# Performance work log

Hardware: AMD Instinct MI355X
Metric: run time of the kernel (lower is better)

Reference implementation:

```python
import jax, jax.numpy as jnp
import numpy as np

CAT_CARDS = [10, 20, 15, 8, 30, 12, 5, 25, 6, 40, 18, 9]   # categorical_card entries with card > 1 (first 20 entries)
NUM = 32          # num_numerical
NBIN = 8          # categorical_card[:-2] entries with card == 1
NLIKE = 2         # last two categorical_card entries, both card 1
NMASK = NUM + len(CAT_CARDS) + NBIN + NLIKE   # 32 + 22 = 54 mask heads
LAT, HID, B = 128, 1024, 16384
TAU = 1.0
EPS = 1e-20


def setup_inputs() -> dict:
    key = jax.random.key(0)
    ks = jax.random.split(key, 7)
    w = lambda k, sh: (jax.random.normal(k, sh, jnp.float32) * 0.02)
    return {
        "z": jax.random.normal(ks[0], (B, LAT), jnp.float32),
        "W1": w(ks[1], (LAT, HID)), "b1": jnp.zeros((HID,), jnp.float32),
        "W_num": w(ks[2], (HID, NUM)), "b_num": jnp.zeros((NUM,), jnp.float32),
        "W_cat": w(ks[3], (HID, sum(CAT_CARDS))), "b_cat": jnp.zeros((sum(CAT_CARDS),), jnp.float32),
        "W_bin": w(ks[4], (HID, NBIN)), "b_bin": jnp.zeros((NBIN,), jnp.float32),
        "W_like": w(ks[5], (HID, NLIKE)), "b_like": jnp.zeros((NLIKE,), jnp.float32),
        "W_mask": w(ks[6], (HID, NMASK)), "b_mask": jnp.zeros((NMASK,), jnp.float32),
    }


def _gumbel_sigmoid(logits, key, tau=TAU):
    # matches torch: noise~U(0,1); g = -log(-log(noise+eps)+eps); sigmoid((logits+g)/tau); hard=False
    u = jax.random.uniform(key, logits.shape, logits.dtype)
    g = -jnp.log(-jnp.log(u + EPS) + EPS)
    return jax.nn.sigmoid((logits + g) / tau)


def reference(z, W1, b1, W_num, b_num, W_cat, b_cat, W_bin, b_bin, W_like, b_like, W_mask, b_mask):
    nk = jax.random.split(jax.random.key(1), 3)
    h = jax.nn.relu(z @ W1 + b1)                       # [B, HID]
    num_out = h @ W_num + b_num                        # [B, NUM]

    cat_logits = h @ W_cat + b_cat                     # [B, sum(cards)] fused GEMM, then split per head
    splits = np.cumsum(CAT_CARDS)[:-1].tolist()
    cat_out = tuple(jnp.split(cat_logits, splits, axis=1))

    # use_gumbel=True, hard=False: binary / likewise / mask heads get gumbel-sigmoid
    bin_out = _gumbel_sigmoid(h @ W_bin + b_bin, nk[0])      # [B, NBIN]
    like_out = _gumbel_sigmoid(h @ W_like + b_like, nk[1])   # [B, NLIKE]
    mask_out = _gumbel_sigmoid(h @ W_mask + b_mask, nk[2])   # [B, NMASK]

    bins = tuple(bin_out[:, i:i + 1] for i in range(NBIN))
    likes = tuple(like_out[:, i:i + 1] for i in range(NLIKE))
    masks = tuple(mask_out[:, i:i + 1] for i in range(NMASK))
    return (num_out,) + cat_out + bins + likes + masks
```

## Files before the change

kernel.cpp:

```cpp
#include <hip/hip_runtime.h>
#include <stdint.h>

#define B_ROWS 16384
#define LATD   128
#define HIDD   1024

typedef __bf16 bf16x8 __attribute__((ext_vector_type(8)));
typedef float  f32x4  __attribute__((ext_vector_type(4)));
typedef float  f32x4v __attribute__((ext_vector_type(4)));
typedef unsigned short ushort8v __attribute__((ext_vector_type(8)));
typedef unsigned int   uint2v   __attribute__((ext_vector_type(2)));

template<int N> __device__ __forceinline__ void waitv() {
  asm volatile("s_waitcnt vmcnt(%0)" :: "i"(N) : "memory");
  __builtin_amdgcn_sched_barrier(0);
}
__device__ __forceinline__ void gl16(bf16x8& r, const unsigned short* p) {
  asm volatile("global_load_dwordx4 %0, %1, off" : "=v"(r) : "v"(p));
}
template<int OFF> __device__ __forceinline__ void gl16o(bf16x8& r, const unsigned short* p) {
  asm volatile("global_load_dwordx4 %0, %1, off offset:%2" : "=v"(r) : "v"(p), "i"(OFF));
}
#define LGKM_BARRIER() do {                                        \
    asm volatile("s_waitcnt lgkmcnt(0)" ::: "memory");             \
    __builtin_amdgcn_s_barrier();                                  \
    asm volatile("" ::: "memory");                                 \
  } while (0)

struct TF2 { unsigned int a, b; };

#define TF_R(x0,x1,r) { x0 += x1; x1 = ((x1 << (r)) | (x1 >> (32 - (r)))); x1 ^= x0; }

__host__ __device__ constexpr TF2 threefry2x32(unsigned k0, unsigned k1, unsigned c0, unsigned c1) {
  unsigned ks2 = k0 ^ k1 ^ 0x1BD11BDAu;
  unsigned x0 = c0 + k0, x1 = c1 + k1;
  TF_R(x0,x1,13) TF_R(x0,x1,15) TF_R(x0,x1,26) TF_R(x0,x1,6)
  x0 += k1;  x1 += ks2 + 1u;
  TF_R(x0,x1,17) TF_R(x0,x1,29) TF_R(x0,x1,16) TF_R(x0,x1,24)
  x0 += ks2; x1 += k0 + 2u;
  TF_R(x0,x1,13) TF_R(x0,x1,15) TF_R(x0,x1,26) TF_R(x0,x1,6)
  x0 += k0;  x1 += k1 + 3u;
  TF_R(x0,x1,17) TF_R(x0,x1,29) TF_R(x0,x1,16) TF_R(x0,x1,24)
  x0 += k1;  x1 += ks2 + 4u;
  TF_R(x0,x1,13) TF_R(x0,x1,15) TF_R(x0,x1,26) TF_R(x0,x1,6)
  x0 += ks2; x1 += k0 + 5u;
  return {x0, x1};
}

constexpr TF2 NK0 = threefry2x32(0u, 1u, 0u, 0u);
constexpr TF2 NK1 = threefry2x32(0u, 1u, 0u, 1u);
constexpr TF2 NK2 = threefry2x32(0u, 1u, 0u, 2u);

__device__ __forceinline__ unsigned short f2bf(float f) {
  unsigned u = __float_as_uint(f);
  return (unsigned short)((u + 0x7fffu + ((u >> 16) & 1u)) >> 16);
}

__global__ __launch_bounds__(256) void prep_kernel(
    const float* __restrict__ W1,
    const float* __restrict__ Wnum, const float* __restrict__ Wcat,
    const float* __restrict__ Wbin, const float* __restrict__ Wlike,
    const float* __restrict__ Wmask,
    const float* __restrict__ bnum, const float* __restrict__ bcat,
    const float* __restrict__ bbin, const float* __restrict__ blike,
    const float* __restrict__ bmask,
    unsigned short* __restrict__ W1p,
    unsigned short* __restrict__ Wallp,
    float* __restrict__ ball) {
  __shared__ __align__(16) unsigned short lds[16 * 136];
  const int b = blockIdx.x, t = threadIdx.x;

  if (b < 64) {
    const int n0 = b * 16;
    const int nq = t & 15;
    float v[8];
    #pragma unroll
    for (int i = 0; i < 8; ++i) {
      int k = i * 16 + (t >> 4);
      v[i] = W1[(size_t)k * HIDD + n0 + nq];
    }
    #pragma unroll
    for (int i = 0; i < 8; ++i) {
      int k = i * 16 + (t >> 4);
      lds[nq * 136 + k] = f2bf(v[i]);
    }
    __syncthreads();
    const int ks = t >> 6, l = t & 63;
    const int l15 = l & 15, l4 = (l >> 4);
    ushort8v p = *(const ushort8v*)(lds + l15 * 136 + ks * 32 + l4 * 8);
    *(ushort8v*)(W1p + ((size_t)(b * 4 + ks) * 64 + l) * 8) = p;
  } else if (b < 224) {
    const int q  = b - 64;
    const int nt = q >> 3, kb = q & 7;
    const int n0 = nt * 16, k0 = kb * 128;
    const int n = n0 + (t & 15);
    const float* src = nullptr; int stride = 0;
    if (n < 32)       { src = Wnum  + n;         stride = 32;  }
    else if (n < 230) { src = Wcat  + (n - 32);  stride = 198; }
    else if (n < 238) { src = Wbin  + (n - 230); stride = 8;   }
    else if (n < 240) { src = Wlike + (n - 238); stride = 2;   }
    else if (n < 294) { src = Wmask + (n - 240); stride = 54;  }
    float v[8];
    if (src) {
      #pragma unroll
      for (int i = 0; i < 8; ++i) {
        int kk_loc = i * 16 + (t >> 4);
        v[i] = src[(size_t)(k0 + kk_loc) * stride];
      }
    } else {
      #pragma unroll
      for (int i = 0; i < 8; ++i) v[i] = 0.f;
    }
    #pragma unroll
    for (int i = 0; i < 8; ++i) {
      int kk_loc = i * 16 + (t >> 4);
      lds[(t & 15) * 136 + kk_loc] = f2bf(v[i]);
    }
    __syncthreads();
    const int kt_loc = t >> 6, l = t & 63;
    const int l15 = l & 15, l4 = (l >> 4);
    ushort8v p = *(const ushort8v*)(lds + l15 * 136 + kt_loc * 32 + l4 * 8);
    const int g = nt * 32 + kb * 4 + kt_loc;
    *(ushort8v*)(Wallp + ((size_t)g * 64 + l) * 8) = p;
  } else {
    for (int n = t; n < 320; n += 256) {
      float v = 0.f;
      if (n < 32)       v = bnum [n];
      else if (n < 230) v = bcat [n - 32];
      else if (n < 238) v = bbin [n - 230];
      else if (n < 240) v = blike[n - 238];
      else if (n < 294) v = bmask[n - 240];
      ball[n] = v;
    }
  }
}

template<int G>
__device__ __forceinline__ void run_phases(
    const int w, const int lane, const int l15, const int l4, const int nt0,
    const unsigned short* __restrict__ W1p, const unsigned short* __restrict__ Wallp,
    const float* __restrict__ b1,
    unsigned char* smem, f32x4 (&acc)[4][3]) {

  unsigned short* zs = (unsigned short*)smem;
  unsigned char* hbase  = smem + 17408;
  unsigned char* mytile = hbase + w * 16384;

  f32x4 hb1[8];
  #pragma unroll
  for (int ct = 0; ct < 8; ++ct)
    hb1[ct] = *(const f32x4*)(b1 + w * 128 + ct * 16 + l4 * 4);

  bf16x8 za[4][4];
  #pragma unroll
  for (int rt = 0; rt < 4; ++rt)
    #pragma unroll
    for (int ks = 0; ks < 4; ++ks)
      za[rt][ks] = *(const bf16x8*)(zs + (rt * 16 + l15) * 136 + ks * 32 + l4 * 8);

  bf16x8 wq1[2][4];
  const unsigned short* w1b = W1p + (size_t)w * 16384 + lane * 8;
  #pragma unroll
  for (int ct = 0; ct < 2; ++ct) {
    const unsigned short* p = w1b + ct * 2048;
    gl16o<0>(wq1[ct][0], p); gl16o<1024>(wq1[ct][1], p);
    gl16o<2048>(wq1[ct][2], p); gl16o<3072>(wq1[ct][3], p);
  }

  bf16x8 wq2[4][G];
  const unsigned short* w2b = Wallp + lane * 8;

  #pragma unroll
  for (int ct = 0; ct < 8; ++ct) {
    if (ct < 7) waitv<4>();
    else        waitv<G * 4>();
    f32x4 a[4] = {};
    #pragma unroll
    for (int ks = 0; ks < 4; ++ks)
      #pragma unroll
      for (int rt = 0; rt < 4; ++rt)
        a[rt] = __builtin_amdgcn_mfma_f32_16x16x32_bf16(wq1[ct & 1][ks], za[rt][ks], a[rt], 0, 0, 0);
    #pragma unroll
    for (int rt = 0; rt < 4; ++rt) {
      float v0 = fmaxf(a[rt][0] + hb1[ct][0], 0.f);
      float v1 = fmaxf(a[rt][1] + hb1[ct][1], 0.f);
      float v2 = fmaxf(a[rt][2] + hb1[ct][2], 0.f);
      float v3 = fmaxf(a[rt][3] + hb1[ct][3], 0.f);
      uint2v u;
      u[0] = (unsigned)f2bf(v0) | ((unsigned)f2bf(v1) << 16);
      u[1] = (unsigned)f2bf(v2) | ((unsigned)f2bf(v3) << 16);
      const int byte = ((ct >> 1) * 4 + rt) * 1024
                     + ((ct & 1) * 2 + (l4 >> 1)) * 256
                     + l15 * 16 + (l4 & 1) * 8;
      *(uint2v*)(mytile + byte) = u;
    }
    if (ct < 6) {
      const unsigned short* p = w1b + (ct + 2) * 2048;
      gl16o<0>(wq1[ct & 1][0], p); gl16o<1024>(wq1[ct & 1][1], p);
      gl16o<2048>(wq1[ct & 1][2], p); gl16o<3072>(wq1[ct & 1][3], p);
    } else if (ct == 6) {
      #pragma unroll
      for (int g = 0; g < 4; ++g)
        #pragma unroll
        for (int cc = 0; cc < G; ++cc)
          gl16(wq2[g][cc], w2b + (size_t)((nt0 + cc) * 32 + g) * 512);
    }
  }

  LGKM_BARRIER();

  #pragma unroll
  for (int rt = 0; rt < 4; ++rt)
    #pragma unroll
    for (int ct = 0; ct < 3; ++ct)
      acc[rt][ct] = (f32x4){0.f, 0.f, 0.f, 0.f};

  #pragma unroll
  for (int g = 0; g < 32; ++g) {
    if (g < 29)       waitv<G * 3>();
    else if (g == 29) waitv<G * 2>();
    else if (g == 30) waitv<G>();
    else              waitv<0>();
    const unsigned char* hc = hbase + (g >> 2) * 16384 + (g & 3) * 4096 + lane * 16;
    #pragma unroll
    for (int rt = 0; rt < 4; ++rt) {
      bf16x8 ha = *(const bf16x8*)(hc + rt * 1024);
      #pragma unroll
      for (int ct = 0; ct < G; ++ct)
        acc[rt][ct] = __builtin_amdgcn_mfma_f32_16x16x32_bf16(ha, wq2[g & 3][ct], acc[rt][ct], 0, 0, 0);
    }
    if (g + 4 < 32) {
      #pragma unroll
      for (int cc = 0; cc < G; ++cc)
        gl16(wq2[g & 3][cc], w2b + (size_t)((nt0 + cc) * 32 + (g + 4)) * 512);
    }
  }
}

__global__ __launch_bounds__(512, 2) void decoder_kernel(
    const float* __restrict__ z, const float* __restrict__ b1,
    const unsigned short* __restrict__ W1p, const unsigned short* __restrict__ Wallp,
    const float* __restrict__ ball, float* __restrict__ out) {
  __shared__ __align__(16) unsigned char smem[148480];
  unsigned short* zs = (unsigned short*)smem;
  float* outs = (float*)smem;

  const int tid  = threadIdx.x;
  const int lane = tid & 63;
  const int w    = tid >> 6;
  const int l15  = lane & 15;
  const int l4   = lane >> 4;
  const int r0   = blockIdx.x * 64;

  #pragma unroll
  for (int it = 0; it < 2; ++it) {
    int ch  = tid + it * 512;
    int row = ch >> 4;
    int k0  = (ch & 15) * 8;
    const float* src = z + (size_t)(r0 + row) * LATD + k0;
    f32x4v f0 = __builtin_nontemporal_load((const f32x4v*)src);
    f32x4v f1 = __builtin_nontemporal_load((const f32x4v*)(src + 4));
    ushort8v p;
    p[0] = f2bf(f0[0]); p[1] = f2bf(f0[1]); p[2] = f2bf(f0[2]); p[3] = f2bf(f0[3]);
    p[4] = f2bf(f1[0]); p[5] = f2bf(f1[1]); p[6] = f2bf(f1[2]); p[7] = f2bf(f1[3]);
    *(ushort8v*)(zs + row * 136 + k0) = p;
  }
  __syncthreads();

  const int cb  = (w < 4) ? w * 48 : 192 + (w - 4) * 32;
  const int nt0 = (w < 4) ? w * 3  : 12 + (w - 4) * 2;
  const int myG = (w < 4) ? 3 : 2;

  f32x4 acc[4][3];
  if (w < 4) run_phases<3>(w, lane, l15, l4, nt0, W1p, Wallp, b1, smem, acc);
  else       run_phases<2>(w, lane, l15, l4, nt0, W1p, Wallp, b1, smem, acc);

  __syncthreads();

  #pragma unroll
  for (int ct = 0; ct < 3; ++ct) {
    if (ct < myG) {
      float b2 = ball[cb + ct * 16 + l15];
      #pragma unroll
      for (int rt = 0; rt < 4; ++rt)
        #pragma unroll
        for (int j = 0; j < 4; ++j)
          outs[(rt * 16 + l4 * 4 + j) * 321 + cb + ct * 16 + l15] = acc[rt][ct][j] + b2;
    }
  }
  __syncthreads();

  {
    constexpr int cards[13] = {32,10,20,15,8,30,12,5,25,6,40,18,9};
    constexpr int cbase[13] = {0,32,42,62,77,85,115,127,132,157,163,203,221};
    #pragma unroll
    for (int blk = 0; blk < 13; ++blk) {
      const int card = cards[blk];
      const int cbs  = cbase[blk];
      float* gout = out + (size_t)B_ROWS * cbs + (size_t)r0 * card;
      for (int v = tid; v < card * 16; v += 512) {
        int gg = v * 4;
        f32x4v vbuf;
        #pragma unroll
        for (int e = 0; e < 4; ++e) {
          int ge = gg + e;
          int brow = ge / card;
          int j = ge - brow * card;
          vbuf[e] = outs[brow * 321 + cbs + j];
        }
        __builtin_nontemporal_store(vbuf, (f32x4v*)(gout + gg));
      }
    }
  }

  {
    int c = 230 + (tid >> 3);
    unsigned ka, kb; int Nh, head;
    if (c < 238)      { ka = NK0.a; kb = NK0.b; Nh = 8;  head = c - 230; }
    else if (c < 240) { ka = NK1.a; kb = NK1.b; Nh = 2;  head = c - 238; }
    else              { ka = NK2.a; kb = NK2.b; Nh = 54; head = c - 240; }
    #pragma unroll
    for (int q = 0; q < 2; ++q) {
      int rq = (tid & 7) * 4 + q * 32;
      f32x4v vbuf;
      #pragma unroll
      for (int e = 0; e < 4; ++e) {
        int rl = rq + e;
        float x = outs[rl * 321 + c];
        unsigned j = (unsigned)((r0 + rl) * Nh + head);
        TF2 t = threefry2x32(ka, kb, 0u, j);
        unsigned bits = t.a ^ t.b;
        float u  = __uint_as_float((bits >> 9) | 0x3f800000u) - 1.0f;
        float gn = -__logf(-__logf(u + 1e-20f) + 1e-20f);
        vbuf[e] = 1.0f / (1.0f + __expf(-(x + gn)));
      }
      __builtin_nontemporal_store(vbuf, (f32x4v*)(out + (size_t)B_ROWS * c + r0 + rq));
    }
  }
}

extern "C" void kernel_launch(void* const* d_in, const int* in_sizes, int n_in,
                              void* d_out, int out_size, void* d_ws, size_t ws_size,
                              hipStream_t stream) {
  const float* z     = (const float*)d_in[0];
  const float* W1    = (const float*)d_in[1];
  const float* b1    = (const float*)d_in[2];
  const float* Wnum  = (const float*)d_in[3];
  const float* bnum  = (const float*)d_in[4];
  const float* Wcat  = (const float*)d_in[5];
  const float* bcat  = (const float*)d_in[6];
  const float* Wbin  = (const float*)d_in[7];
  const float* bbin  = (const float*)d_in[8];
  const float* Wlike = (const float*)d_in[9];
  const float* blike = (const float*)d_in[10];
  const float* Wmask = (const float*)d_in[11];
  const float* bmask = (const float*)d_in[12];

  unsigned short* W1p   = (unsigned short*)d_ws;
  unsigned short* Wallp = W1p + 131072;
  float*          ball  = (float*)(Wallp + 327680);

  prep_kernel<<<225, 256, 0, stream>>>(
      W1, Wnum, Wcat, Wbin, Wlike, Wmask, bnum, bcat, bbin, blike, bmask,
      W1p, Wallp, ball);

  decoder_kernel<<<B_ROWS / 64, 512, 0, stream>>>(
      z, b1, W1p, Wallp, ball, (float*)d_out);
}
```

Measured before the change: 29.33 us.

## Split second GEMM across warps by K halves with LDS reduction

The second GEMM's 320 output columns were split unevenly across 8 warps (3 or 2 column tiles each). Now 4 column groups each own 5 tiles, and the two warp halves each take half of the K dimension. The partial sums are combined through shared memory: one half writes with bias and the other adds after a barrier. This balances MFMA work across warps and halves each warp's K loop. In exchange it adds register pressure from 20 accumulators and 20 prefetch registers, plus an extra barrier and an LDS read-modify-write pass.

```diff
diff --git a/kernel.cpp b/kernel.cpp
--- a/kernel.cpp
+++ b/kernel.cpp
@@ -135,15 +135,43 @@
   }
 }
 
-template<int G>
-__device__ __forceinline__ void run_phases(
-    const int w, const int lane, const int l15, const int l4, const int nt0,
+__global__ __launch_bounds__(512, 2) void decoder_kernel(
+    const float* __restrict__ z, const float* __restrict__ b1,
     const unsigned short* __restrict__ W1p, const unsigned short* __restrict__ Wallp,
-    const float* __restrict__ b1,
-    unsigned char* smem, f32x4 (&acc)[4][3]) {
-
+    const float* __restrict__ ball, float* __restrict__ out) {
+  __shared__ __align__(16) unsigned char smem[148480];
   unsigned short* zs = (unsigned short*)smem;
-  unsigned char* hbase  = smem + 17408;
+  unsigned char* hbase = smem + 17408;
+  float* outs = (float*)smem;
+
+  const int tid  = threadIdx.x;
+  const int lane = tid & 63;
+  const int w    = tid >> 6;
+  const int wc   = w & 3;
+  const int wk   = w >> 2;
+  const int l15  = lane & 15;
+  const int l4   = lane >> 4;
+  const int r0   = blockIdx.x * 64;
+
+  #pragma unroll
+  for (int it = 0; it < 2; ++it) {
+    int ch  = tid + it * 512;
+    int row = ch >> 4;
+    int k0  = (ch & 15) * 8;
+    const float* src = z + (size_t)(r0 + row) * LATD + k0;
+    f32x4v f0 = __builtin_nontemporal_load((const f32x4v*)src);
+    f32x4v f1 = __builtin_nontemporal_load((const f32x4v*)(src + 4));
+    ushort8v p;
+    p[0] = f2bf(f0[0]); p[1] = f2bf(f0[1]); p[2] = f2bf(f0[2]); p[3] = f2bf(f0[3]);
+    p[4] = f2bf(f1[0]); p[5] = f2bf(f1[1]); p[6] = f2bf(f1[2]); p[7] = f2bf(f1[3]);
+    *(ushort8v*)(zs + row * 136 + k0) = p;
+  }
+  __syncthreads();
+
+  const int cb  = wc * 80;
+  const int nt0 = wc * 5;
+  const int kt0 = wk * 16;
+
   unsigned char* mytile = hbase + w * 16384;
 
   f32x4 hb1[8];
@@ -167,13 +195,13 @@
     gl16o<2048>(wq1[ct][2], p); gl16o<3072>(wq1[ct][3], p);
   }
 
-  bf16x8 wq2[4][G];
+  bf16x8 wq2[4][5];
   const unsigned short* w2b = Wallp + lane * 8;
 
   #pragma unroll
   for (int ct = 0; ct < 8; ++ct) {
     if (ct < 7) waitv<4>();
-    else        waitv<G * 4>();
+    else        waitv<20>();
     f32x4 a[4] = {};
     #pragma unroll
     for (int ks = 0; ks < 4; ++ks)
@@ -202,84 +230,48 @@
       #pragma unroll
       for (int g = 0; g < 4; ++g)
         #pragma unroll
-        for (int cc = 0; cc < G; ++cc)
-          gl16(wq2[g][cc], w2b + (size_t)((nt0 + cc) * 32 + g) * 512);
+        for (int cc = 0; cc < 5; ++cc)
+          gl16(wq2[g][cc], w2b + (size_t)((nt0 + cc) * 32 + kt0 + g) * 512);
     }
   }
 
   LGKM_BARRIER();
 
+  f32x4 acc[4][5];
   #pragma unroll
   for (int rt = 0; rt < 4; ++rt)
     #pragma unroll
-    for (int ct = 0; ct < 3; ++ct)
+    for (int ct = 0; ct < 5; ++ct)
       acc[rt][ct] = (f32x4){0.f, 0.f, 0.f, 0.f};
 
   #pragma unroll
-  for (int g = 0; g < 32; ++g) {
-    if (g < 29)       waitv<G * 3>();
-    else if (g == 29) waitv<G * 2>();
-    else if (g == 30) waitv<G>();
-    else              waitv<0>();
-    const unsigned char* hc = hbase + (g >> 2) * 16384 + (g & 3) * 4096 + lane * 16;
+  for (int g = 0; g < 16; ++g) {
+    const int rem = 15 - g;
+    if (rem >= 3)      waitv<15>();
+    else if (rem == 2) waitv<10>();
+    else if (rem == 1) waitv<5>();
+    else               waitv<0>();
+    const int kt = kt0 + g;
+    const unsigned char* hc = hbase + (kt >> 2) * 16384 + (kt & 3) * 4096 + lane * 16;
     #pragma unroll
     for (int rt = 0; rt < 4; ++rt) {
       bf16x8 ha = *(const bf16x8*)(hc + rt * 1024);
       #pragma unroll
-      for (int ct = 0; ct < G; ++ct)
+      for (int ct = 0; ct < 5; ++ct)
         acc[rt][ct] = __builtin_amdgcn_mfma_f32_16x16x32_bf16(ha, wq2[g & 3][ct], acc[rt][ct], 0, 0, 0);
     }
-    if (g + 4 < 32) {
-      #pragma unroll
-      for (int cc = 0; cc < G; ++cc)
-        gl16(wq2[g & 3][cc], w2b + (size_t)((nt0 + cc) * 32 + (g + 4)) * 512);
-    }
-  }
-}
-
-__global__ __launch_bounds__(512, 2) void decoder_kernel(
-    const float* __restrict__ z, const float* __restrict__ b1,
-    const unsigned short* __restrict__ W1p, const unsigned short* __restrict__ Wallp,
-    const float* __restrict__ ball, float* __restrict__ out) {
-  __shared__ __align__(16) unsigned char smem[148480];
-  unsigned short* zs = (unsigned short*)smem;
-  float* outs = (float*)smem;
-
-  const int tid  = threadIdx.x;
-  const int lane = tid & 63;
-  const int w    = tid >> 6;
-  const int l15  = lane & 15;
-  const int l4   = lane >> 4;
-  const int r0   = blockIdx.x * 64;
-
-  #pragma unroll
-  for (int it = 0; it < 2; ++it) {
-    int ch  = tid + it * 512;
-    int row = ch >> 4;
-    int k0  = (ch & 15) * 8;
-    const float* src = z + (size_t)(r0 + row) * LATD + k0;
-    f32x4v f0 = __builtin_nontemporal_load((const f32x4v*)src);
-    f32x4v f1 = __builtin_nontemporal_load((const f32x4v*)(src + 4));
-    ushort8v p;
-    p[0] = f2bf(f0[0]); p[1] = f2bf(f0[1]); p[2] = f2bf(f0[2]); p[3] = f2bf(f0[3]);
-    p[4] = f2bf(f1[0]); p[5] = f2bf(f1[1]); p[6] = f2bf(f1[2]); p[7] = f2bf(f1[3]);
-    *(ushort8v*)(zs + row * 136 + k0) = p;
-  }
+    if (g + 4 < 16) {
+      #pragma unroll
+      for (int cc = 0; cc < 5; ++cc)
+        gl16(wq2[g & 3][cc], w2b + (size_t)((nt0 + cc) * 32 + kt0 + g + 4) * 512);
+    }
+  }
+
   __syncthreads();
 
-  const int cb  = (w < 4) ? w * 48 : 192 + (w - 4) * 32;
-  const int nt0 = (w < 4) ? w * 3  : 12 + (w - 4) * 2;
-  const int myG = (w < 4) ? 3 : 2;
-
-  f32x4 acc[4][3];
-  if (w < 4) run_phases<3>(w, lane, l15, l4, nt0, W1p, Wallp, b1, smem, acc);
-  else       run_phases<2>(w, lane, l15, l4, nt0, W1p, Wallp, b1, smem, acc);
-
-  __syncthreads();
-
-  #pragma unroll
-  for (int ct = 0; ct < 3; ++ct) {
-    if (ct < myG) {
+  if (wk == 0) {
+    #pragma unroll
+    for (int ct = 0; ct < 5; ++ct) {
       float b2 = ball[cb + ct * 16 + l15];
       #pragma unroll
       for (int rt = 0; rt < 4; ++rt)
@@ -287,6 +279,16 @@
         for (int j = 0; j < 4; ++j)
           outs[(rt * 16 + l4 * 4 + j) * 321 + cb + ct * 16 + l15] = acc[rt][ct][j] + b2;
     }
+  }
+  __syncthreads();
+  if (wk == 1) {
+    #pragma unroll
+    for (int ct = 0; ct < 5; ++ct)
+      #pragma unroll
+      for (int rt = 0; rt < 4; ++rt)
+        #pragma unroll
+        for (int j = 0; j < 4; ++j)
+          outs[(rt * 16 + l4 * 4 + j) * 321 + cb + ct * 16 + l15] += acc[rt][ct][j];
   }
   __syncthreads();
 
```

Result: slower. 30.56 us (+4.2%).
